# Kernel tuning notes

Hardware: AMD Instinct MI355X
Metric: run time of the kernel (lower is better)

Reference implementation:

```python
import jax, jax.numpy as jnp
import numpy as np
import math

NUM_BUCKETS = 32
MAX_DISTANCE = 128
N_HEADS = 16
D_KV = 64


def _relative_position_bucket(relative_position, num_buckets=NUM_BUCKETS, max_distance=MAX_DISTANCE):
    # bidirectional (encoder) variant
    num_buckets //= 2
    relative_buckets = (relative_position > 0).astype(jnp.int32) * num_buckets
    rp = jnp.abs(relative_position)
    max_exact = num_buckets // 2
    is_small = rp < max_exact
    rp_large = max_exact + (
        jnp.log(jnp.maximum(rp, 1).astype(jnp.float32) / max_exact)
        / math.log(max_distance / max_exact)
        * (num_buckets - max_exact)
    ).astype(jnp.int32)
    rp_large = jnp.minimum(rp_large, num_buckets - 1)
    return relative_buckets + jnp.where(is_small, rp, rp_large)


def compute_bias(rel_bias, q_len, k_len):
    ctx = jnp.arange(q_len)[:, None]
    mem = jnp.arange(k_len)[None, :]
    buckets = _relative_position_bucket(mem - ctx)          # [q, k]
    values = rel_bias[buckets]                               # [q, k, h]
    return jnp.transpose(values, (2, 0, 1))[None]            # [1, h, q, k]


def setup_inputs() -> dict:
    key = jax.random.key(0)
    ks = jax.random.split(key, 6)
    d_model, inner = 1024, N_HEADS * D_KV
    s = 0.02
    return {
        "hidden_states": jax.random.normal(ks[0], (2, 2048, d_model), jnp.float32),
        "Wq": jax.random.normal(ks[1], (d_model, inner), jnp.float32) * s,
        "Wk": jax.random.normal(ks[2], (d_model, inner), jnp.float32) * s,
        "Wv": jax.random.normal(ks[3], (d_model, inner), jnp.float32) * s,
        "Wo": jax.random.normal(ks[4], (inner, d_model), jnp.float32) * s,
        "rel_bias": jax.random.normal(ks[5], (NUM_BUCKETS, N_HEADS), jnp.float32) * s,
    }


def reference(hidden_states, Wq, Wk, Wv, Wo, rel_bias):
    B, S, D = hidden_states.shape

    def split_heads(x):  # [B,S,inner] -> [B,H,S,dk]
        return x.reshape(B, S, N_HEADS, D_KV).transpose(0, 2, 1, 3)

    q = split_heads(hidden_states @ Wq)
    k = split_heads(hidden_states @ Wk)
    v = split_heads(hidden_states @ Wv)

    # T5 does NOT scale by 1/sqrt(d_kv)
    scores = jnp.einsum("bhqd,bhkd->bhqk", q, k)
    scores = scores + compute_bias(rel_bias, S, S)
    attn = jax.nn.softmax(scores, axis=-1)
    ctx = jnp.einsum("bhqk,bhkd->bhqd", attn, v)
    ctx = ctx.transpose(0, 2, 1, 3).reshape(B, S, N_HEADS * D_KV)
    return ctx @ Wo
```

## Files before the change

kernel.cpp:

```cpp
#include <hip/hip_runtime.h>
#include <hip/hip_bf16.h>

typedef __bf16 bf16x8 __attribute__((ext_vector_type(8)));
typedef __bf16 bf16x4 __attribute__((ext_vector_type(4)));
typedef float floatx4 __attribute__((ext_vector_type(4)));
typedef float floatx16 __attribute__((ext_vector_type(16)));
using bf16 = __hip_bfloat16;

#define S_    2048
#define NHEAD 16
#define LOG2E 1.4426950408889634f

__device__ __forceinline__ void load_lds16(const bf16* g, void* lds) {
  __builtin_amdgcn_global_load_lds((const __attribute__((address_space(1))) void*)g,
                                   (__attribute__((address_space(3))) void*)lds, 16, 0, 0);
}

__global__ void prep_kernel(const float* __restrict__ hidden,
                            const float* __restrict__ wq, const float* __restrict__ wk,
                            const float* __restrict__ wv, const float* __restrict__ wo,
                            const float* __restrict__ rel_bias,
                            bf16* __restrict__ hbf, bf16* __restrict__ wt_qkv,
                            bf16* __restrict__ wt_o, float* __restrict__ tab) {
  __shared__ bf16 tile[32][33];
  int bid = blockIdx.x;
  if (bid < 4096) {
    int i = (bid * 256 + threadIdx.x) * 4;
    float4 v = *(const float4*)(hidden + i);
    bf16 o[4] = {__float2bfloat16(v.x), __float2bfloat16(v.y),
                 __float2bfloat16(v.z), __float2bfloat16(v.w)};
    *(uint2*)(hbf + i) = *(const uint2*)o;
  } else if (bid < 8192) {
    int r = bid - 4096;
    int mat = r >> 10;
    int rem = r & 1023;
    int n0 = (rem & 31) * 32, k0 = (rem >> 5) * 32;
    int tx = threadIdx.x & 31, ty = threadIdx.x >> 5;
    const float* src = (mat == 0) ? wq : (mat == 1) ? wk : (mat == 2) ? wv : wo;
    bf16* dst = (mat == 3) ? wt_o : wt_qkv + mat * 1024 * 1024;
#pragma unroll
    for (int j = 0; j < 32; j += 8)
      tile[ty + j][tx] = __float2bfloat16(src[(k0 + ty + j) * 1024 + n0 + tx]);
    __syncthreads();
#pragma unroll
    for (int j = 0; j < 32; j += 8)
      dst[(n0 + ty + j) * 1024 + k0 + tx] = tile[tx][ty + j];
  } else {
    int idx = (bid - 8192) * 256 + threadIdx.x;
    int h = idx >> 12, j = idx & 4095;
    int delta = j - 2048;
    int rb = (delta > 0) ? 16 : 0;
    int rpa = delta < 0 ? -delta : delta;
    int bsmall;
    if (rpa < 8) {
      bsmall = rpa;
    } else {
      int lg = 25 - __clz(rpa * rpa);
      bsmall = 8 + lg;
      if (bsmall > 15) bsmall = 15;
    }
    tab[idx] = rel_bias[(rb + bsmall) * 16 + h] * LOG2E;
  }
}

__global__ __launch_bounds__(256) void gemm_qkv_kernel(const bf16* __restrict__ A,
                                                       const bf16* __restrict__ Bt,
                                                       bf16* __restrict__ qh,
                                                       bf16* __restrict__ kf,
                                                       bf16* __restrict__ vf) {
  const int K = 1024;
  __shared__ bf16 As[128 * 32];
  __shared__ bf16 Bs[128 * 32];
  int t = threadIdx.x;
  int m0 = blockIdx.y * 128, n0 = blockIdx.x * 128;
  int w = t >> 6, lane = t & 63, ln = lane & 15, quad = lane >> 4;
  int wr = w >> 1, wc = w & 1;
  floatx4 acc[4][4];
  floatx4 zero = {0.f, 0.f, 0.f, 0.f};
#pragma unroll
  for (int i = 0; i < 4; i++)
#pragma unroll
    for (int j = 0; j < 4; j++) acc[i][j] = zero;

  int r = t >> 2, c = (t & 3) * 8;
  const bf16* Ag = A + (long)(m0 + r) * K + c;
  const bf16* Bg = Bt + (long)(n0 + r) * K + c;
  char* ldsA0 = (char*)As + w * 1024;
  char* ldsA1 = ldsA0 + 4096;
  char* ldsB0 = (char*)Bs + w * 1024;
  char* ldsB1 = ldsB0 + 4096;

  for (int k0 = 0; k0 < K; k0 += 32) {
    load_lds16(Ag + k0, ldsA0);
    load_lds16(Ag + (long)64 * K + k0, ldsA1);
    load_lds16(Bg + k0, ldsB0);
    load_lds16(Bg + (long)64 * K + k0, ldsB1);
    __syncthreads();
    bf16x8 af[4], bfv[4];
#pragma unroll
    for (int i = 0; i < 4; i++)
      af[i] = *(const bf16x8*)&As[(wr * 64 + i * 16 + ln) * 32 + quad * 8];
#pragma unroll
    for (int j = 0; j < 4; j++)
      bfv[j] = *(const bf16x8*)&Bs[(wc * 64 + j * 16 + ln) * 32 + quad * 8];
#pragma unroll
    for (int i = 0; i < 4; i++)
#pragma unroll
      for (int j = 0; j < 4; j++)
        acc[i][j] = __builtin_amdgcn_mfma_f32_16x16x32_bf16(af[i], bfv[j], acc[i][j], 0, 0, 0);
    __syncthreads();
  }

  int nb = n0 + wc * 64;
  int type = nb >> 10, h = (nb >> 6) & 15;
  int b = (m0 >> 11);
  int sl0 = (m0 & 2047) + wr * 64;
  long bhbase = (long)((b * 16 + h)) * 131072;

  if (type == 0) {
#pragma unroll
    for (int i = 0; i < 4; i++)
#pragma unroll
      for (int j = 0; j < 4; j++) {
        int d = j * 16 + ln;
#pragma unroll
        for (int rr = 0; rr < 4; rr++) {
          int s = sl0 + i * 16 + quad * 4 + rr;
          qh[bhbase + (long)s * 64 + d] = __float2bfloat16(acc[i][j][rr]);
        }
      }
  } else if (type == 1) {
#pragma unroll
    for (int i = 0; i < 4; i++)
#pragma unroll
      for (int j = 0; j < 4; j++) {
        long base = bhbase + sl0 * 64 + (i >> 1) * 2048 + j * 512 + (ln >> 3) * 256 +
                    (i & 1) * 128 + quad * 32 + (ln & 7);
#pragma unroll
        for (int rr = 0; rr < 4; rr++)
          kf[base + rr * 8] = __float2bfloat16(acc[i][j][rr]);
      }
  } else {
#pragma unroll
    for (int i = 0; i < 4; i++)
#pragma unroll
      for (int j = 0; j < 4; j++) {
        long off = sl0 * 64 + i * 1024 + (j >> 1) * 512 + (quad >> 1) * 256 +
                   ((j & 1) * 16 + ln) * 8 + (quad & 1) * 4;
        bf16x4 pk = {(__bf16)acc[i][j][0], (__bf16)acc[i][j][1],
                     (__bf16)acc[i][j][2], (__bf16)acc[i][j][3]};
        *(bf16x4*)(vf + bhbase + off) = pk;
      }
  }
}

#define LOADKV(Kr, Vr, kk)                                        \
  {                                                               \
    const bf16* kp = kfb + (kk) * 64 + loff;                      \
    const bf16* vp = vfb + (kk) * 64 + loff;                      \
    Kr[0] = *(const bf16x8*)(kp);                                 \
    Kr[1] = *(const bf16x8*)(kp + 512);                           \
    Kr[2] = *(const bf16x8*)(kp + 1024);                          \
    Kr[3] = *(const bf16x8*)(kp + 1536);                          \
    Vr[0] = *(const bf16x8*)(vp);                                 \
    Vr[1] = *(const bf16x8*)(vp + 512);                           \
    Vr[2] = *(const bf16x8*)(vp + 1024);                          \
    Vr[3] = *(const bf16x8*)(vp + 1536);                          \
  }

#define COMPUTE(Kr, Vr, kk)                                                       \
  {                                                                               \
    floatx16 st = zf;                                                             \
    __builtin_amdgcn_s_setprio(1);                                                \
    st = __builtin_amdgcn_mfma_f32_32x32x16_bf16(Kr[0], Qf[0], st, 0, 0, 0);      \
    st = __builtin_amdgcn_mfma_f32_32x32x16_bf16(Kr[1], Qf[1], st, 0, 0, 0);      \
    st = __builtin_amdgcn_mfma_f32_32x32x16_bf16(Kr[2], Qf[2], st, 0, 0, 0);      \
    st = __builtin_amdgcn_mfma_f32_32x32x16_bf16(Kr[3], Qf[3], st, 0, 0, 0);      \
    __builtin_amdgcn_s_setprio(0);                                                \
    float p[16];                                                                  \
    bool near = ((kk) > qw - 160) && ((kk) < qw + 160);                           \
    if (near) {                                                                   \
      int kb = (kk) + 4 * h5 - (qw + l31) + 2048;                                 \
      _Pragma("unroll")                                                           \
      for (int r = 0; r < 16; r++)                                                \
        p[r] = __builtin_amdgcn_exp2f(                                            \
            fmaf(st[r], LOG2E, bt[kb + (r & 3) + 8 * (r >> 2)]));                 \
    } else {                                                                      \
      float cb = ((kk) > qw) ? cpos : cneg;                                       \
      _Pragma("unroll")                                                           \
      for (int r = 0; r < 16; r++)                                                \
        p[r] = __builtin_amdgcn_exp2f(fmaf(st[r], LOG2E, cb));                    \
    }                                                                             \
    float a0 = (p[0] + p[1]) + (p[2] + p[3]);                                     \
    float a1 = (p[4] + p[5]) + (p[6] + p[7]);                                     \
    float a2 = (p[8] + p[9]) + (p[10] + p[11]);                                   \
    float a3 = (p[12] + p[13]) + (p[14] + p[15]);                                 \
    l_acc += (a0 + a1) + (a2 + a3);                                               \
    unsigned d[8];                                                                \
    _Pragma("unroll")                                                             \
    for (int i = 0; i < 8; i++)                                                   \
      asm("v_cvt_pk_bf16_f32 %0, %1, %2" : "=v"(d[i]) : "v"(p[2*i]), "v"(p[2*i+1])); \
    unsigned w0 = d[0], w2 = d[2];                                                \
    asm("v_permlane32_swap_b32 %0, %1" : "+v"(w0), "+v"(w2));                     \
    unsigned w1 = d[1], w3 = d[3];                                                \
    asm("v_permlane32_swap_b32 %0, %1" : "+v"(w1), "+v"(w3));                     \
    unsigned w4 = d[4], w6 = d[6];                                                \
    asm("v_permlane32_swap_b32 %0, %1" : "+v"(w4), "+v"(w6));                     \
    unsigned w5 = d[5], w7 = d[7];                                                \
    asm("v_permlane32_swap_b32 %0, %1" : "+v"(w5), "+v"(w7));                     \
    union { unsigned u[4]; bf16x8 v; } a0u, a1u;                                  \
    a0u.u[0] = w0; a0u.u[1] = w1; a0u.u[2] = w2; a0u.u[3] = w3;                   \
    a1u.u[0] = w4; a1u.u[1] = w5; a1u.u[2] = w6; a1u.u[3] = w7;                   \
    __builtin_amdgcn_s_setprio(1);                                                \
    o0 = __builtin_amdgcn_mfma_f32_32x32x16_bf16(a0u.v, Vr[0], o0, 0, 0, 0);      \
    o1 = __builtin_amdgcn_mfma_f32_32x32x16_bf16(a0u.v, Vr[1], o1, 0, 0, 0);      \
    o0 = __builtin_amdgcn_mfma_f32_32x32x16_bf16(a1u.v, Vr[2], o0, 0, 0, 0);      \
    o1 = __builtin_amdgcn_mfma_f32_32x32x16_bf16(a1u.v, Vr[3], o1, 0, 0, 0);      \
    __builtin_amdgcn_s_setprio(0);                                                \
  }

__global__ __launch_bounds__(256, 2) void attn_kernel(const bf16* __restrict__ qh,
                                                      const bf16* __restrict__ kf,
                                                      const bf16* __restrict__ vf,
                                                      const float* __restrict__ btab,
                                                      bf16* __restrict__ ctx) {
  int t = threadIdx.x, w = t >> 6, lane = t & 63;
  int l31 = lane & 31, h5 = lane >> 5;

  int lin = blockIdx.x;
  int xcd = lin & 7, j = lin >> 3;
  int bh = xcd * 4 + (j >> 4);
  int qblk = j & 15;
  int b = bh >> 4, h = bh & 15;
  int qw = qblk * 128 + w * 32;

  const bf16* qbase = qh + (long)bh * S_ * 64;
  const bf16* kfb = kf + (long)bh * S_ * 64;
  const bf16* vfb = vf + (long)bh * S_ * 64;
  const float* bt = btab + h * 4096;
  int loff = h5 * 256 + l31 * 8;

  bf16x8 Qf[4];
#pragma unroll
  for (int ds = 0; ds < 4; ds++)
    Qf[ds] = *(const bf16x8*)(qbase + (long)(qw + l31) * 64 + ds * 16 + h5 * 8);

  float cneg = bt[0], cpos = bt[4095];
  float l_acc = 0.f;
  floatx16 zf = {0.f, 0.f, 0.f, 0.f, 0.f, 0.f, 0.f, 0.f,
                 0.f, 0.f, 0.f, 0.f, 0.f, 0.f, 0.f, 0.f};
  floatx16 o0 = zf, o1 = zf;

  bf16x8 Ka[4], Va[4], Kb[4], Vb[4];
  LOADKV(Ka, Va, 0);
  LOADKV(Kb, Vb, 32);

  for (int k0 = 0; k0 < S_; k0 += 64) {
    COMPUTE(Ka, Va, k0);
    if (k0 + 64 < S_) LOADKV(Ka, Va, k0 + 64);
    COMPUTE(Kb, Vb, k0 + 32);
    if (k0 + 96 < S_) LOADKV(Kb, Vb, k0 + 96);
  }

  l_acc += __shfl_xor(l_acc, 32);
  float linv = 1.0f / l_acc;
#pragma unroll
  for (int r = 0; r < 16; r++) {
    int qrow = (r & 3) + 8 * (r >> 2) + 4 * h5;
    float lv = __shfl(linv, qrow);
    int q = qw + qrow;
    long base = (long)(b * S_ + q) * 1024 + h * 64 + l31;
    ctx[base] = __float2bfloat16(o0[r] * lv);
    ctx[base + 32] = __float2bfloat16(o1[r] * lv);
  }
}

__global__ __launch_bounds__(256) void gemm_bt_kernel(const bf16* __restrict__ A,
                                                      const bf16* __restrict__ Bt,
                                                      float* __restrict__ C,
                                                      int M, int N, int K) {
  __shared__ bf16 As[64 * 32];
  __shared__ bf16 Bs[128 * 32];
  int t = threadIdx.x;
  int m0 = blockIdx.y * 64, n0 = blockIdx.x * 128;
  int w = t >> 6, lane = t & 63, ln = lane & 15, quad = lane >> 4;
  int wr = w & 1, wc = w >> 1;
  floatx4 acc[2][4];
  floatx4 zero = {0.f, 0.f, 0.f, 0.f};
#pragma unroll
  for (int i = 0; i < 2; i++)
#pragma unroll
    for (int j = 0; j < 4; j++) acc[i][j] = zero;

  int r = t >> 2, c = (t & 3) * 8;
  const bf16* Ag = A + (long)(m0 + r) * K + c;
  const bf16* Bg = Bt + (long)(n0 + r) * K + c;
  char* ldsA0 = (char*)As + w * 1024;
  char* ldsB0 = (char*)Bs + w * 1024;
  char* ldsB1 = ldsB0 + 4096;

  for (int k0 = 0; k0 < K; k0 += 32) {
    load_lds16(Ag + k0, ldsA0);
    load_lds16(Bg + k0, ldsB0);
    load_lds16(Bg + (long)64 * K + k0, ldsB1);
    __syncthreads();
    bf16x8 af[2], bfv[4];
#pragma unroll
    for (int i = 0; i < 2; i++)
      af[i] = *(const bf16x8*)&As[(wr * 32 + i * 16 + ln) * 32 + quad * 8];
#pragma unroll
    for (int j = 0; j < 4; j++)
      bfv[j] = *(const bf16x8*)&Bs[(wc * 64 + j * 16 + ln) * 32 + quad * 8];
#pragma unroll
    for (int i = 0; i < 2; i++)
#pragma unroll
      for (int j = 0; j < 4; j++)
        acc[i][j] = __builtin_amdgcn_mfma_f32_16x16x32_bf16(af[i], bfv[j], acc[i][j], 0, 0, 0);
    __syncthreads();
  }

#pragma unroll
  for (int i = 0; i < 2; i++)
#pragma unroll
    for (int j = 0; j < 4; j++)
#pragma unroll
      for (int rr = 0; rr < 4; rr++)
        C[(long)(m0 + wr * 32 + i * 16 + quad * 4 + rr) * N + n0 + wc * 64 + j * 16 + ln] =
            acc[i][j][rr];
}

extern "C" void kernel_launch(void* const* d_in, const int* in_sizes, int n_in,
                              void* d_out, int out_size, void* d_ws, size_t ws_size,
                              hipStream_t stream) {
  (void)in_sizes; (void)n_in; (void)out_size; (void)ws_size;
  const float* hidden   = (const float*)d_in[0];
  const float* Wq       = (const float*)d_in[1];
  const float* Wk       = (const float*)d_in[2];
  const float* Wv       = (const float*)d_in[3];
  const float* Wo       = (const float*)d_in[4];
  const float* rel_bias = (const float*)d_in[5];

  char* ws = (char*)d_ws;
  bf16*  hbf    = (bf16*)(ws + 0);
  bf16*  wt_qkv = (bf16*)(ws + 8388608);
  bf16*  wt_o   = (bf16*)(ws + 14680064);
  float* btab   = (float*)(ws + 16777216);
  bf16*  qh     = (bf16*)(ws + 17039360);
  bf16*  kf     = (bf16*)(ws + 25427968);
  bf16*  vf     = (bf16*)(ws + 33816576);
  bf16*  ctx    = (bf16*)(ws + 42205184);

  prep_kernel<<<dim3(8448), dim3(256), 0, stream>>>(hidden, Wq, Wk, Wv, Wo, rel_bias,
                                                    hbf, wt_qkv, wt_o, btab);
  gemm_qkv_kernel<<<dim3(24, 32), dim3(256), 0, stream>>>(hbf, wt_qkv, qh, kf, vf);
  attn_kernel<<<dim3(512), dim3(256), 0, stream>>>(qh, kf, vf, btab, ctx);
  gemm_bt_kernel<<<dim3(8, 64), dim3(256), 0, stream>>>(ctx, wt_o, (float*)d_out, 4096, 1024, 1024);
}
```

Measured before the change: 188.4 us.

## Swizzle QKV GEMM LDS with BK=64 and batch QK MFMAs before softmax

The QKV projection GEMM now stages 64-wide K slices, halving the number of barriers per tile, and uses an XOR swizzle on the LDS column slot to avoid bank conflicts on fragment reads. In the attention kernel, both 32-key QK^T MFMA clusters are issued back to back under raised priority. The next K tiles are then loaded before the exp/PV work for each half, splitting K and V prefetch so loads overlap the softmax. This raises register pressure (two live score accumulators) and doubles the GEMM's LDS footprint, which may lower occupancy.

```diff
diff --git a/kernel.cpp b/kernel.cpp
--- a/kernel.cpp
+++ b/kernel.cpp
@@ -69,8 +69,8 @@
                                                        bf16* __restrict__ kf,
                                                        bf16* __restrict__ vf) {
   const int K = 1024;
-  __shared__ bf16 As[128 * 32];
-  __shared__ bf16 Bs[128 * 32];
+  __shared__ bf16 As[128 * 64];
+  __shared__ bf16 Bs[128 * 64];
   int t = threadIdx.x;
   int m0 = blockIdx.y * 128, n0 = blockIdx.x * 128;
   int w = t >> 6, lane = t & 63, ln = lane & 15, quad = lane >> 4;
@@ -82,32 +82,34 @@
 #pragma unroll
     for (int j = 0; j < 4; j++) acc[i][j] = zero;
 
-  int r = t >> 2, c = (t & 3) * 8;
-  const bf16* Ag = A + (long)(m0 + r) * K + c;
-  const bf16* Bg = Bt + (long)(n0 + r) * K + c;
-  char* ldsA0 = (char*)As + w * 1024;
-  char* ldsA1 = ldsA0 + 4096;
-  char* ldsB0 = (char*)Bs + w * 1024;
-  char* ldsB1 = ldsB0 + 4096;
-
-  for (int k0 = 0; k0 < K; k0 += 32) {
-    load_lds16(Ag + k0, ldsA0);
-    load_lds16(Ag + (long)64 * K + k0, ldsA1);
-    load_lds16(Bg + k0, ldsB0);
-    load_lds16(Bg + (long)64 * K + k0, ldsB1);
-    __syncthreads();
-    bf16x8 af[4], bfv[4];
-#pragma unroll
-    for (int i = 0; i < 4; i++)
-      af[i] = *(const bf16x8*)&As[(wr * 64 + i * 16 + ln) * 32 + quad * 8];
-#pragma unroll
-    for (int j = 0; j < 4; j++)
-      bfv[j] = *(const bf16x8*)&Bs[(wc * 64 + j * 16 + ln) * 32 + quad * 8];
-#pragma unroll
-    for (int i = 0; i < 4; i++)
+  int r = t >> 3, c8 = t & 7;
+  int cs = (c8 ^ (r & 7)) * 8;
+  const bf16* Ag = A + (long)(m0 + r) * K + cs;
+  const bf16* Bg = Bt + (long)(n0 + r) * K + cs;
+
+  for (int k0 = 0; k0 < K; k0 += 64) {
+#pragma unroll
+    for (int ch = 0; ch < 4; ch++) {
+      load_lds16(Ag + (long)ch * 32 * K + k0, (char*)As + ch * 4096 + w * 1024);
+      load_lds16(Bg + (long)ch * 32 * K + k0, (char*)Bs + ch * 4096 + w * 1024);
+    }
+    __syncthreads();
+#pragma unroll
+    for (int s = 0; s < 2; s++) {
+      int slot = ((s * 4 + quad) ^ (ln & 7)) * 8;
+      bf16x8 af[4], bfv[4];
+#pragma unroll
+      for (int i = 0; i < 4; i++)
+        af[i] = *(const bf16x8*)&As[(wr * 64 + i * 16 + ln) * 64 + slot];
 #pragma unroll
       for (int j = 0; j < 4; j++)
-        acc[i][j] = __builtin_amdgcn_mfma_f32_16x16x32_bf16(af[i], bfv[j], acc[i][j], 0, 0, 0);
+        bfv[j] = *(const bf16x8*)&Bs[(wc * 64 + j * 16 + ln) * 64 + slot];
+#pragma unroll
+      for (int i = 0; i < 4; i++)
+#pragma unroll
+        for (int j = 0; j < 4; j++)
+          acc[i][j] = __builtin_amdgcn_mfma_f32_16x16x32_bf16(af[i], bfv[j], acc[i][j], 0, 0, 0);
+    }
     __syncthreads();
   }
 
@@ -154,29 +156,34 @@
   }
 }
 
-#define LOADKV(Kr, Vr, kk)                                        \
+#define LOADK(Kr, kk)                                             \
   {                                                               \
     const bf16* kp = kfb + (kk) * 64 + loff;                      \
-    const bf16* vp = vfb + (kk) * 64 + loff;                      \
     Kr[0] = *(const bf16x8*)(kp);                                 \
     Kr[1] = *(const bf16x8*)(kp + 512);                           \
     Kr[2] = *(const bf16x8*)(kp + 1024);                          \
     Kr[3] = *(const bf16x8*)(kp + 1536);                          \
+  }
+
+#define LOADV(Vr, kk)                                             \
+  {                                                               \
+    const bf16* vp = vfb + (kk) * 64 + loff;                      \
     Vr[0] = *(const bf16x8*)(vp);                                 \
     Vr[1] = *(const bf16x8*)(vp + 512);                           \
     Vr[2] = *(const bf16x8*)(vp + 1024);                          \
     Vr[3] = *(const bf16x8*)(vp + 1536);                          \
   }
 
-#define COMPUTE(Kr, Vr, kk)                                                       \
+#define QKCLUSTER(stv, Kr)                                                        \
   {                                                                               \
-    floatx16 st = zf;                                                             \
-    __builtin_amdgcn_s_setprio(1);                                                \
-    st = __builtin_amdgcn_mfma_f32_32x32x16_bf16(Kr[0], Qf[0], st, 0, 0, 0);      \
-    st = __builtin_amdgcn_mfma_f32_32x32x16_bf16(Kr[1], Qf[1], st, 0, 0, 0);      \
-    st = __builtin_amdgcn_mfma_f32_32x32x16_bf16(Kr[2], Qf[2], st, 0, 0, 0);      \
-    st = __builtin_amdgcn_mfma_f32_32x32x16_bf16(Kr[3], Qf[3], st, 0, 0, 0);      \
-    __builtin_amdgcn_s_setprio(0);                                                \
+    stv = __builtin_amdgcn_mfma_f32_32x32x16_bf16(Kr[0], Qf[0], stv, 0, 0, 0);    \
+    stv = __builtin_amdgcn_mfma_f32_32x32x16_bf16(Kr[1], Qf[1], stv, 0, 0, 0);    \
+    stv = __builtin_amdgcn_mfma_f32_32x32x16_bf16(Kr[2], Qf[2], stv, 0, 0, 0);    \
+    stv = __builtin_amdgcn_mfma_f32_32x32x16_bf16(Kr[3], Qf[3], stv, 0, 0, 0);    \
+  }
+
+#define FINISH(stv, Vr, kk)                                                       \
+  {                                                                               \
     float p[16];                                                                  \
     bool near = ((kk) > qw - 160) && ((kk) < qw + 160);                           \
     if (near) {                                                                   \
@@ -184,12 +191,12 @@
       _Pragma("unroll")                                                           \
       for (int r = 0; r < 16; r++)                                                \
         p[r] = __builtin_amdgcn_exp2f(                                            \
-            fmaf(st[r], LOG2E, bt[kb + (r & 3) + 8 * (r >> 2)]));                 \
+            fmaf(stv[r], LOG2E, bt[kb + (r & 3) + 8 * (r >> 2)]));                \
     } else {                                                                      \
       float cb = ((kk) > qw) ? cpos : cneg;                                       \
       _Pragma("unroll")                                                           \
       for (int r = 0; r < 16; r++)                                                \
-        p[r] = __builtin_amdgcn_exp2f(fmaf(st[r], LOG2E, cb));                    \
+        p[r] = __builtin_amdgcn_exp2f(fmaf(stv[r], LOG2E, cb));                   \
     }                                                                             \
     float a0 = (p[0] + p[1]) + (p[2] + p[3]);                                     \
     float a1 = (p[4] + p[5]) + (p[6] + p[7]);                                     \
@@ -252,14 +259,21 @@
   floatx16 o0 = zf, o1 = zf;
 
   bf16x8 Ka[4], Va[4], Kb[4], Vb[4];
-  LOADKV(Ka, Va, 0);
-  LOADKV(Kb, Vb, 32);
+  LOADK(Ka, 0);  LOADV(Va, 0);
+  LOADK(Kb, 32); LOADV(Vb, 32);
 
   for (int k0 = 0; k0 < S_; k0 += 64) {
-    COMPUTE(Ka, Va, k0);
-    if (k0 + 64 < S_) LOADKV(Ka, Va, k0 + 64);
-    COMPUTE(Kb, Vb, k0 + 32);
-    if (k0 + 96 < S_) LOADKV(Kb, Vb, k0 + 96);
+    floatx16 sa = zf, sb = zf;
+    __builtin_amdgcn_s_setprio(1);
+    QKCLUSTER(sa, Ka);
+    QKCLUSTER(sb, Kb);
+    __builtin_amdgcn_s_setprio(0);
+    if (k0 + 64 < S_) LOADK(Ka, k0 + 64);
+    if (k0 + 96 < S_) LOADK(Kb, k0 + 96);
+    FINISH(sa, Va, k0);
+    if (k0 + 64 < S_) LOADV(Va, k0 + 64);
+    FINISH(sb, Vb, k0 + 32);
+    if (k0 + 96 < S_) LOADV(Vb, k0 + 96);
   }
 
   l_acc += __shfl_xor(l_acc, 32);
```

Measured after the change: 190.2 us. About the same (+1.0%).

## Double-buffer QKV GEMM with 256x256 tiles and swizzled LDS

Applied to the files above, without the earlier changes.

Rewrites the QKV projection GEMM to use 256x256 output tiles with 512 threads, a K-step of 64, and a two-stage double-buffered LDS pipeline fed by direct global-to-LDS loads, synchronized with vmcnt waits. LDS columns are XOR-swizzled to avoid bank conflicts, and MFMA sections are wrapped in setprio to favour the math wavefronts. The aim is to hide global load latency and raise data reuse per tile. In exchange, the grid drops to 192 blocks and each block uses 128KB of LDS, which may leave some CUs idle and limit occupancy.

```diff
diff --git a/kernel.cpp b/kernel.cpp
--- a/kernel.cpp
+++ b/kernel.cpp
@@ -63,63 +63,88 @@
   }
 }
 
-__global__ __launch_bounds__(256) void gemm_qkv_kernel(const bf16* __restrict__ A,
+__global__ __launch_bounds__(512) void gemm_qkv_kernel(const bf16* __restrict__ A,
                                                        const bf16* __restrict__ Bt,
                                                        bf16* __restrict__ qh,
                                                        bf16* __restrict__ kf,
                                                        bf16* __restrict__ vf) {
   const int K = 1024;
-  __shared__ bf16 As[128 * 32];
-  __shared__ bf16 Bs[128 * 32];
+  __shared__ char lds[131072];
   int t = threadIdx.x;
-  int m0 = blockIdx.y * 128, n0 = blockIdx.x * 128;
+  int m0 = blockIdx.y * 256, n0 = blockIdx.x * 256;
   int w = t >> 6, lane = t & 63, ln = lane & 15, quad = lane >> 4;
-  int wr = w >> 1, wc = w & 1;
-  floatx4 acc[4][4];
+  int wm = w >> 2, wn = w & 3;
+  floatx4 acc[8][4];
   floatx4 zero = {0.f, 0.f, 0.f, 0.f};
 #pragma unroll
-  for (int i = 0; i < 4; i++)
+  for (int i = 0; i < 8; i++)
 #pragma unroll
     for (int j = 0; j < 4; j++) acc[i][j] = zero;
 
-  int r = t >> 2, c = (t & 3) * 8;
-  const bf16* Ag = A + (long)(m0 + r) * K + c;
-  const bf16* Bg = Bt + (long)(n0 + r) * K + c;
-  char* ldsA0 = (char*)As + w * 1024;
-  char* ldsA1 = ldsA0 + 4096;
-  char* ldsB0 = (char*)Bs + w * 1024;
-  char* ldsB1 = ldsB0 + 4096;
-
-  for (int k0 = 0; k0 < K; k0 += 32) {
-    load_lds16(Ag + k0, ldsA0);
-    load_lds16(Ag + (long)64 * K + k0, ldsA1);
-    load_lds16(Bg + k0, ldsB0);
-    load_lds16(Bg + (long)64 * K + k0, ldsB1);
-    __syncthreads();
-    bf16x8 af[4], bfv[4];
-#pragma unroll
-    for (int i = 0; i < 4; i++)
-      af[i] = *(const bf16x8*)&As[(wr * 64 + i * 16 + ln) * 32 + quad * 8];
-#pragma unroll
-    for (int j = 0; j < 4; j++)
-      bfv[j] = *(const bf16x8*)&Bs[(wc * 64 + j * 16 + ln) * 32 + quad * 8];
-#pragma unroll
-    for (int i = 0; i < 4; i++)
+  int r = t >> 3, c8 = t & 7;
+  int cs = (c8 ^ (r & 7)) * 8;
+  const bf16* Ag = A + (long)(m0 + r) * K + cs;
+  const bf16* Bg = Bt + (long)(n0 + r) * K + cs;
+
+#define QKV_STAGE(bufi, kt)                                                     \
+  {                                                                             \
+    char* ab = lds + (bufi) * 65536;                                            \
+    char* bb = ab + 32768;                                                      \
+    int kk = (kt) * 64;                                                         \
+    _Pragma("unroll")                                                           \
+    for (int ch = 0; ch < 4; ch++) {                                            \
+      load_lds16(Ag + (long)ch * 64 * K + kk, ab + ch * 8192 + t * 16);         \
+      load_lds16(Bg + (long)ch * 64 * K + kk, bb + ch * 8192 + t * 16);         \
+    }                                                                           \
+  }
+
+  QKV_STAGE(0, 0);
+  QKV_STAGE(1, 1);
+  asm volatile("s_waitcnt vmcnt(8)" ::: "memory");
+  __builtin_amdgcn_s_barrier();
+
+  for (int kt = 0; kt < 16; ++kt) {
+    const bf16* As_ = (const bf16*)(lds + (kt & 1) * 65536);
+    const bf16* Bs_ = As_ + 16384;
+#pragma unroll
+    for (int s = 0; s < 2; s++) {
+      int slot = ((s * 4 + quad) ^ (ln & 7)) * 8;
+      bf16x8 af[8], bfv[4];
+#pragma unroll
+      for (int i = 0; i < 8; i++)
+        af[i] = *(const bf16x8*)&As_[(wm * 128 + i * 16 + ln) * 64 + slot];
 #pragma unroll
       for (int j = 0; j < 4; j++)
-        acc[i][j] = __builtin_amdgcn_mfma_f32_16x16x32_bf16(af[i], bfv[j], acc[i][j], 0, 0, 0);
-    __syncthreads();
-  }
-
-  int nb = n0 + wc * 64;
+        bfv[j] = *(const bf16x8*)&Bs_[(wn * 64 + j * 16 + ln) * 64 + slot];
+      __builtin_amdgcn_s_setprio(1);
+#pragma unroll
+      for (int i = 0; i < 8; i++)
+#pragma unroll
+        for (int j = 0; j < 4; j++)
+          acc[i][j] = __builtin_amdgcn_mfma_f32_16x16x32_bf16(af[i], bfv[j], acc[i][j], 0, 0, 0);
+      __builtin_amdgcn_s_setprio(0);
+    }
+    if (kt == 15) break;
+    __builtin_amdgcn_s_barrier();
+    if (kt + 2 < 16) {
+      QKV_STAGE(kt & 1, kt + 2);
+      asm volatile("s_waitcnt vmcnt(8)" ::: "memory");
+    } else {
+      asm volatile("s_waitcnt vmcnt(0)" ::: "memory");
+    }
+    __builtin_amdgcn_s_barrier();
+  }
+#undef QKV_STAGE
+
+  int nb = n0 + wn * 64;
   int type = nb >> 10, h = (nb >> 6) & 15;
   int b = (m0 >> 11);
-  int sl0 = (m0 & 2047) + wr * 64;
+  int sl0 = (m0 & 2047) + wm * 128;
   long bhbase = (long)((b * 16 + h)) * 131072;
 
   if (type == 0) {
 #pragma unroll
-    for (int i = 0; i < 4; i++)
+    for (int i = 0; i < 8; i++)
 #pragma unroll
       for (int j = 0; j < 4; j++) {
         int d = j * 16 + ln;
@@ -131,7 +156,7 @@
       }
   } else if (type == 1) {
 #pragma unroll
-    for (int i = 0; i < 4; i++)
+    for (int i = 0; i < 8; i++)
 #pragma unroll
       for (int j = 0; j < 4; j++) {
         long base = bhbase + sl0 * 64 + (i >> 1) * 2048 + j * 512 + (ln >> 3) * 256 +
@@ -142,7 +167,7 @@
       }
   } else {
 #pragma unroll
-    for (int i = 0; i < 4; i++)
+    for (int i = 0; i < 8; i++)
 #pragma unroll
       for (int j = 0; j < 4; j++) {
         long off = sl0 * 64 + i * 1024 + (j >> 1) * 512 + (quad >> 1) * 256 +
@@ -352,7 +377,7 @@
 
   prep_kernel<<<dim3(8448), dim3(256), 0, stream>>>(hidden, Wq, Wk, Wv, Wo, rel_bias,
                                                     hbf, wt_qkv, wt_o, btab);
-  gemm_qkv_kernel<<<dim3(24, 32), dim3(256), 0, stream>>>(hbf, wt_qkv, qh, kf, vf);
+  gemm_qkv_kernel<<<dim3(12, 16), dim3(512), 0, stream>>>(hbf, wt_qkv, qh, kf, vf);
   attn_kernel<<<dim3(512), dim3(256), 0, stream>>>(qh, kf, vf, btab, ctx);
   gemm_bt_kernel<<<dim3(8, 64), dim3(256), 0, stream>>>(ctx, wt_o, (float*)d_out, 4096, 1024, 1024);
 }
```

After: 187.8 us. No clear change (-0.3%).
